# Performance work log

Measured on AMD Instinct MI355X. Metric: run time of the kernel, lower is better.

The kernel has to match this reference:

```python
import jax, jax.numpy as jnp
import numpy as np
from math import atanh

B, T, D_IN, H = 16, 1024, 512, 1024
INIT_A = atanh(0.95)


def setup_inputs() -> dict:
    key = jax.random.key(0)
    k1, k2, k3, k4 = jax.random.split(key, 4)
    x = jax.random.normal(k1, (B, T, D_IN), dtype=jnp.float32)
    h0 = jax.random.normal(k2, (B, H), dtype=jnp.float32)
    # raw_a initialized near atanh(0.95) as in the module, with small jitter
    raw_a = INIT_A + 0.01 * jax.random.normal(k3, (H,), dtype=jnp.float32)
    # xavier-uniform for W_x.weight [H, D_IN]
    limit = float(np.sqrt(6.0 / (D_IN + H)))
    W = jax.random.uniform(k4, (H, D_IN), dtype=jnp.float32, minval=-limit, maxval=limit)
    b = jnp.zeros((H,), dtype=jnp.float32)
    return {"x": x, "h0": h0, "raw_a": raw_a, "W": W, "b": b}


def reference(x, h0, raw_a, W, b):
    # h_t = a * h_{t-1} + W x_t + b, computed via cumprod/cumsum parallel-scan trick
    a = jnp.tanh(raw_a)                                   # [H] (rho is None)
    z = jnp.einsum('btd,hd->bth', x, W) + b               # [B,T,H]
    A = jnp.broadcast_to(a, (x.shape[1], a.shape[0]))     # [T,H]
    p = jnp.cumprod(A, axis=0)[None]                      # [1,T,H], p[t] = a^(t+1)
    v = jnp.cumsum(z / jnp.maximum(p, 1e-12), axis=1)     # [B,T,H]
    h = v * p + p * h0[:, None, :]                        # include initial state
    zero_mask = (jnp.abs(a) < 1e-6)[None, None, :]        # degenerate a ~ 0 channels
    h = jnp.where(zero_mask, z, h)
    return h
```

## Files before the change

### kernel.cpp

```cpp
#include <hip/hip_runtime.h>
#include <cstdint>

#define B_DIM 16
#define T_DIM 1024
#define DK    512
#define H_DIM 1024
#define CCH   16
#define LCH   64

typedef __bf16 bf16x8 __attribute__((ext_vector_type(8)));
typedef __bf16 bf16x4 __attribute__((ext_vector_type(4)));
typedef float  f32x4  __attribute__((ext_vector_type(4)));

typedef __attribute__((address_space(1))) unsigned int* as1p;
typedef __attribute__((address_space(3))) unsigned int* as3p;

__device__ __forceinline__ void async_cp16(const void* g, void* l) {
  __builtin_amdgcn_global_load_lds((as1p)(uint64_t)g,
                                   (as3p)(uint32_t)(uint64_t)l, 16, 0, 0);
}

__global__ __launch_bounds__(256) void cvt_f32_bf16(const float* __restrict__ in,
                                                    __bf16* __restrict__ out, int n4) {
  int i = blockIdx.x * 256 + threadIdx.x;
  if (i >= n4) return;
  f32x4 v = ((const f32x4*)in)[i];
  bf16x4 o;
  o.x = (__bf16)v.x; o.y = (__bf16)v.y; o.z = (__bf16)v.z; o.w = (__bf16)v.w;
  ((bf16x4*)out)[i] = o;
}

__global__ __launch_bounds__(256) void compute_meta(const float* __restrict__ raw_a,
                                                    float4* __restrict__ meta) {
  int h = blockIdx.x * 256 + threadIdx.x;
  if (h >= H_DIM) return;
  float a = tanhf(raw_a[h]);
  float la2 = log2f(fabsf(a));
  meta[h] = make_float4(a, la2, (a < 0.f) ? 1.f : 0.f, (fabsf(a) < 1e-6f) ? 1.f : 0.f);
}

__global__ __launch_bounds__(256) void gemm_bt(const __bf16* __restrict__ A,
                                               const __bf16* __restrict__ Bw,
                                               const float* __restrict__ bias,
                                               const float4* __restrict__ meta,
                                               float* __restrict__ C,
                                               float* __restrict__ S) {
  constexpr int N = H_DIM;
  constexpr int K = DK;

  __shared__ __align__(16) __bf16 As[128 * 32];
  __shared__ __align__(16) __bf16 Bs[128 * 32];
  __shared__ float sred[2][128];

  const int tid  = threadIdx.x;
  const int wave = tid >> 6;
  const int lane = tid & 63;
  const int m0 = blockIdx.y * 128;
  const int n0 = blockIdx.x * 128;
  const int wm = wave >> 1;
  const int wn = wave & 1;

  const int lrow = lane >> 2;
  const int lk   = (lane & 3) * 8;

  f32x4 acc[4][4];
#pragma unroll
  for (int i = 0; i < 4; ++i)
#pragma unroll
    for (int j = 0; j < 4; ++j) acc[i][j] = (f32x4){0.f, 0.f, 0.f, 0.f};

  for (int k0 = 0; k0 < K; k0 += 32) {
    __syncthreads();
#pragma unroll
    for (int q = 0; q < 2; ++q) {
      const int rbase = q * 64 + wave * 16;
      const __bf16* ga = A  + (size_t)(m0 + rbase + lrow) * K + k0 + lk;
      async_cp16(ga, As + rbase * 32);
      const __bf16* gb = Bw + (size_t)(n0 + rbase + lrow) * K + k0 + lk;
      async_cp16(gb, Bs + rbase * 32);
    }
    __syncthreads();
#pragma unroll
    for (int i = 0; i < 4; ++i) {
      const bf16x8 af = *(const bf16x8*)(As + (wm * 64 + i * 16 + (lane & 15)) * 32 + (lane >> 4) * 8);
#pragma unroll
      for (int j = 0; j < 4; ++j) {
        const bf16x8 bf = *(const bf16x8*)(Bs + (wn * 64 + j * 16 + (lane & 15)) * 32 + (lane >> 4) * 8);
        acc[i][j] = __builtin_amdgcn_mfma_f32_16x16x32_bf16(af, bf, acc[i][j], 0, 0, 0);
      }
    }
  }

  const int cl = lane & 15;
  const int rq = (lane >> 4) * 4;
  const int b = m0 >> 10;
  const int tloc0 = m0 & 1023;
#pragma unroll
  for (int j = 0; j < 4; ++j) {
    const int col = n0 + wn * 64 + j * 16 + cl;
    const float bv = bias[col];
    const float4 mt = meta[col];
    const float la2 = mt.y;
    const bool neg = mt.z != 0.f;
    float ssum = 0.f;
#pragma unroll
    for (int i = 0; i < 4; ++i) {
      const int rowg = wm * 64 + i * 16 + rq;
#pragma unroll
      for (int r = 0; r < 4; ++r) {
        const int tp1 = tloc0 + rowg + r + 1;
        const float zf = acc[i][j][r] + bv;
        C[(size_t)(m0 + rowg + r) * N + col] = zf;
        float inv = fminf(__builtin_amdgcn_exp2f(-la2 * (float)tp1), 1e12f);
        if (neg && (tp1 & 1)) inv = 1e12f;
        ssum += zf * inv;
      }
    }
    ssum += __shfl_xor(ssum, 16, 64);
    ssum += __shfl_xor(ssum, 32, 64);
    if ((lane >> 4) == 0) sred[wm][wn * 64 + j * 16 + cl] = ssum;
  }
  __syncthreads();
  {
    const int g = tid >> 7;
    const int col = tid & 127;
    S[((size_t)b * CCH + (tloc0 >> 6) + g) * H_DIM + n0 + col] = sred[g][col];
  }
}

__global__ __launch_bounds__(256) void scan_pass2(const float* __restrict__ z,
                                                  const float4* __restrict__ meta,
                                                  const float* __restrict__ S,
                                                  const float* __restrict__ h0,
                                                  float* __restrict__ out) {
  const int h = blockIdx.x * 256 + threadIdx.x;
  const int c = blockIdx.y;
  const int b = blockIdx.z;
  float prefix = 0.f;
  for (int cc = 0; cc < c; ++cc) prefix += S[((size_t)b * CCH + cc) * H_DIM + h];
  const float4 mt = meta[h];
  const float la2 = mt.y;
  const bool neg = mt.z != 0.f;
  const bool zm  = mt.w != 0.f;
  const float h0v = h0[(size_t)b * H_DIM + h];
  float v = prefix;
  const int t0 = c * LCH;
  const size_t base = ((size_t)b * T_DIM + t0) * H_DIM + h;
  for (int t = 0; t < LCH; ++t) {
    const float zt = z[base + (size_t)t * H_DIM];
    const int tp1 = t0 + t + 1;
    float pv = __builtin_amdgcn_exp2f(la2 * (float)tp1);
    if (neg && (tp1 & 1)) pv = -pv;
    const float pc = fmaxf(pv, 1e-12f);
    v += zt * __builtin_amdgcn_rcpf(pc);
    const float hv = v * pv + pv * h0v;
    out[base + (size_t)t * H_DIM] = zm ? zt : hv;
  }
}

extern "C" void kernel_launch(void* const* d_in, const int* in_sizes, int n_in,
                              void* d_out, int out_size, void* d_ws, size_t ws_size,
                              hipStream_t stream) {
  const float* x     = (const float*)d_in[0];
  const float* h0    = (const float*)d_in[1];
  const float* raw_a = (const float*)d_in[2];
  const float* W     = (const float*)d_in[3];
  const float* bias  = (const float*)d_in[4];
  float* out = (float*)d_out;

  char* ws = (char*)d_ws;
  float*  z    = (float*)(ws);
  __bf16* xb   = (__bf16*)(ws + 67108864);
  __bf16* wb   = (__bf16*)(ws + 67108864 + 16777216);
  float4* meta = (float4*)(ws + 67108864 + 16777216 + 1048576);
  float*  S    = (float*)(ws + 67108864 + 16777216 + 1048576 + 16384);

  cvt_f32_bf16<<<(B_DIM * T_DIM * DK / 4 + 255) / 256, 256, 0, stream>>>(x, xb, B_DIM * T_DIM * DK / 4);
  cvt_f32_bf16<<<(H_DIM * DK / 4 + 255) / 256, 256, 0, stream>>>(W, wb, H_DIM * DK / 4);
  compute_meta<<<H_DIM / 256, 256, 0, stream>>>(raw_a, meta);
  gemm_bt<<<dim3(H_DIM / 128, B_DIM * T_DIM / 128), 256, 0, stream>>>(xb, wb, bias, meta, z, S);
  scan_pass2<<<dim3(H_DIM / 256, CCH, B_DIM), 256, 0, stream>>>(z, meta, S, h0, out);
}
```

Measured before the change: 153.7 us.

## Fuse GEMM and chunked scan into one kernel with in-block carry

Replaces the separate GEMM (which wrote z and chunk sums) and scan pass with a single kernel where each block owns one batch and 32 hidden columns and walks the whole sequence in 256-step chunks, scanning the MFMA accumulators in registers with shuffles and carrying prefix sums through shared memory. This removes the 64 MB z round trip and a kernel launch. In exchange the grid shrinks to 512 blocks with narrow 32-column N tiles, so each block re-streams its x rows with little reuse of W and has a long serial time loop, which may cut MFMA efficiency and parallelism.

```diff
diff --git a/kernel.cpp b/kernel.cpp
--- a/kernel.cpp
+++ b/kernel.cpp
@@ -5,8 +5,6 @@
 #define T_DIM 1024
 #define DK    512
 #define H_DIM 1024
-#define CCH   16
-#define LCH   64
 
 typedef __bf16 bf16x8 __attribute__((ext_vector_type(8)));
 typedef __bf16 bf16x4 __attribute__((ext_vector_type(4)));
@@ -39,122 +37,148 @@
   meta[h] = make_float4(a, la2, (a < 0.f) ? 1.f : 0.f, (fabsf(a) < 1e-6f) ? 1.f : 0.f);
 }
 
-__global__ __launch_bounds__(256) void gemm_bt(const __bf16* __restrict__ A,
-                                               const __bf16* __restrict__ Bw,
-                                               const float* __restrict__ bias,
-                                               const float4* __restrict__ meta,
-                                               float* __restrict__ C,
-                                               float* __restrict__ S) {
-  constexpr int N = H_DIM;
-  constexpr int K = DK;
-
-  __shared__ __align__(16) __bf16 As[128 * 32];
-  __shared__ __align__(16) __bf16 Bs[128 * 32];
-  __shared__ float sred[2][128];
+__global__ __launch_bounds__(256, 2) void fused_rnn(const __bf16* __restrict__ xb,
+                                                    const __bf16* __restrict__ wb,
+                                                    const float* __restrict__ bias,
+                                                    const float4* __restrict__ meta,
+                                                    const float* __restrict__ h0g,
+                                                    float* __restrict__ out) {
+  __shared__ __align__(16) __bf16 As[256 * 32];
+  __shared__ __align__(16) __bf16 Bs[32 * 32];
+  __shared__ float chunkTot[4][32];
+  __shared__ float colCarry[32];
 
   const int tid  = threadIdx.x;
   const int wave = tid >> 6;
   const int lane = tid & 63;
-  const int m0 = blockIdx.y * 128;
-  const int n0 = blockIdx.x * 128;
-  const int wm = wave >> 1;
-  const int wn = wave & 1;
-
-  const int lrow = lane >> 2;
-  const int lk   = (lane & 3) * 8;
-
-  f32x4 acc[4][4];
-#pragma unroll
-  for (int i = 0; i < 4; ++i)
-#pragma unroll
-    for (int j = 0; j < 4; ++j) acc[i][j] = (f32x4){0.f, 0.f, 0.f, 0.f};
-
-  for (int k0 = 0; k0 < K; k0 += 32) {
+  const int q = lane >> 4;
+  const int c = lane & 15;
+
+  const int b    = blockIdx.x & 15;
+  const int n0   = (blockIdx.x >> 4) * 32;
+
+  float bias_j[2], la2_j[2], h0_j[2];
+  bool neg_j[2], zm_j[2];
+#pragma unroll
+  for (int j = 0; j < 2; ++j) {
+    const int col = n0 + j * 16 + c;
+    bias_j[j] = bias[col];
+    const float4 mt = meta[col];
+    la2_j[j] = mt.y;
+    neg_j[j] = mt.z != 0.f;
+    zm_j[j]  = mt.w != 0.f;
+    h0_j[j]  = h0g[(size_t)b * H_DIM + col];
+  }
+
+  if (tid < 32) colCarry[tid] = 0.f;
+
+  const int srow = lane >> 2;
+  const int skof = (lane & 3) * 8;
+
+  for (int mc = 0; mc < 4; ++mc) {
+    const int t0 = mc * 256;
+    const __bf16* Abase = xb + (size_t)(b * T_DIM + t0) * DK;
+
+    f32x4 acc[4][2];
+#pragma unroll
+    for (int i = 0; i < 4; ++i)
+#pragma unroll
+      for (int j = 0; j < 2; ++j) acc[i][j] = (f32x4){0.f, 0.f, 0.f, 0.f};
+
+    for (int k0 = 0; k0 < DK; k0 += 32) {
+      __syncthreads();
+#pragma unroll
+      for (int r = 0; r < 4; ++r) {
+        const int s = wave * 4 + r;
+        const __bf16* ga = Abase + (size_t)(s * 16 + srow) * DK + k0 + skof;
+        async_cp16(ga, As + s * 16 * 32);
+      }
+      if (wave < 2) {
+        const __bf16* gb = wb + (size_t)(n0 + wave * 16 + srow) * DK + k0 + skof;
+        async_cp16(gb, Bs + wave * 16 * 32);
+      }
+      __syncthreads();
+      bf16x8 af[4], bfr[2];
+#pragma unroll
+      for (int i = 0; i < 4; ++i)
+        af[i] = *(const bf16x8*)(As + (wave * 64 + i * 16 + c) * 32 + q * 8);
+#pragma unroll
+      for (int j = 0; j < 2; ++j)
+        bfr[j] = *(const bf16x8*)(Bs + (j * 16 + c) * 32 + q * 8);
+#pragma unroll
+      for (int i = 0; i < 4; ++i)
+#pragma unroll
+        for (int j = 0; j < 2; ++j)
+          acc[i][j] = __builtin_amdgcn_mfma_f32_16x16x32_bf16(af[i], bfr[j], acc[i][j], 0, 0, 0);
+    }
+
+    f32x4 vloc[4][2];
+    float icarry[2] = {0.f, 0.f};
+#pragma unroll
+    for (int i = 0; i < 4; ++i) {
+#pragma unroll
+      for (int j = 0; j < 2; ++j) {
+        const float la2 = la2_j[j];
+        f32x4 w;
+#pragma unroll
+        for (int r = 0; r < 4; ++r) {
+          const int tp1 = t0 + wave * 64 + i * 16 + q * 4 + r + 1;
+          const float z = acc[i][j][r] + bias_j[j];
+          float inv = fminf(__builtin_amdgcn_exp2f(-la2 * (float)tp1), 1e12f);
+          if (neg_j[j] && (tp1 & 1)) inv = 1e12f;
+          w[r] = z * inv;
+        }
+        const float pr0 = w[0];
+        const float pr1 = pr0 + w[1];
+        const float pr2 = pr1 + w[2];
+        const float pr3 = pr2 + w[3];
+        const float x1 = __shfl_xor(pr3, 16, 64);
+        const float x2 = __shfl_xor(pr3, 32, 64);
+        const float x3 = __shfl_xor(pr3, 48, 64);
+        float sq = 0.f;
+        if (q >= 2) sq += x2 + x3;
+        if (q & 1) sq += x1;
+        const float base = icarry[j] + sq;
+        vloc[i][j] = (f32x4){base + pr0, base + pr1, base + pr2, base + pr3};
+        icarry[j] += pr3 + x1 + x2 + x3;
+      }
+    }
+    if (q == 0) {
+#pragma unroll
+      for (int j = 0; j < 2; ++j) chunkTot[wave][j * 16 + c] = icarry[j];
+    }
     __syncthreads();
-#pragma unroll
-    for (int q = 0; q < 2; ++q) {
-      const int rbase = q * 64 + wave * 16;
-      const __bf16* ga = A  + (size_t)(m0 + rbase + lrow) * K + k0 + lk;
-      async_cp16(ga, As + rbase * 32);
-      const __bf16* gb = Bw + (size_t)(n0 + rbase + lrow) * K + k0 + lk;
-      async_cp16(gb, Bs + rbase * 32);
+
+    float cc[2];
+#pragma unroll
+    for (int j = 0; j < 2; ++j) {
+      float s = colCarry[j * 16 + c];
+      for (int w2 = 0; w2 < 4; ++w2)
+        if (w2 < wave) s += chunkTot[w2][j * 16 + c];
+      cc[j] = s;
+    }
+#pragma unroll
+    for (int i = 0; i < 4; ++i) {
+#pragma unroll
+      for (int j = 0; j < 2; ++j) {
+        const float la2 = la2_j[j];
+        const int col = n0 + j * 16 + c;
+#pragma unroll
+        for (int r = 0; r < 4; ++r) {
+          const int tl = t0 + wave * 64 + i * 16 + q * 4 + r;
+          const int tp1 = tl + 1;
+          float pv = __builtin_amdgcn_exp2f(la2 * (float)tp1);
+          if (neg_j[j] && (tp1 & 1)) pv = -pv;
+          const float v = cc[j] + vloc[i][j][r];
+          const float hv = pv * v + pv * h0_j[j];
+          const float zval = acc[i][j][r] + bias_j[j];
+          out[(size_t)(b * T_DIM + tl) * H_DIM + col] = zm_j[j] ? zval : hv;
+        }
+      }
     }
     __syncthreads();
-#pragma unroll
-    for (int i = 0; i < 4; ++i) {
-      const bf16x8 af = *(const bf16x8*)(As + (wm * 64 + i * 16 + (lane & 15)) * 32 + (lane >> 4) * 8);
-#pragma unroll
-      for (int j = 0; j < 4; ++j) {
-        const bf16x8 bf = *(const bf16x8*)(Bs + (wn * 64 + j * 16 + (lane & 15)) * 32 + (lane >> 4) * 8);
-        acc[i][j] = __builtin_amdgcn_mfma_f32_16x16x32_bf16(af, bf, acc[i][j], 0, 0, 0);
-      }
-    }
-  }
-
-  const int cl = lane & 15;
-  const int rq = (lane >> 4) * 4;
-  const int b = m0 >> 10;
-  const int tloc0 = m0 & 1023;
-#pragma unroll
-  for (int j = 0; j < 4; ++j) {
-    const int col = n0 + wn * 64 + j * 16 + cl;
-    const float bv = bias[col];
-    const float4 mt = meta[col];
-    const float la2 = mt.y;
-    const bool neg = mt.z != 0.f;
-    float ssum = 0.f;
-#pragma unroll
-    for (int i = 0; i < 4; ++i) {
-      const int rowg = wm * 64 + i * 16 + rq;
-#pragma unroll
-      for (int r = 0; r < 4; ++r) {
-        const int tp1 = tloc0 + rowg + r + 1;
-        const float zf = acc[i][j][r] + bv;
-        C[(size_t)(m0 + rowg + r) * N + col] = zf;
-        float inv = fminf(__builtin_amdgcn_exp2f(-la2 * (float)tp1), 1e12f);
-        if (neg && (tp1 & 1)) inv = 1e12f;
-        ssum += zf * inv;
-      }
-    }
-    ssum += __shfl_xor(ssum, 16, 64);
-    ssum += __shfl_xor(ssum, 32, 64);
-    if ((lane >> 4) == 0) sred[wm][wn * 64 + j * 16 + cl] = ssum;
-  }
-  __syncthreads();
-  {
-    const int g = tid >> 7;
-    const int col = tid & 127;
-    S[((size_t)b * CCH + (tloc0 >> 6) + g) * H_DIM + n0 + col] = sred[g][col];
-  }
-}
-
-__global__ __launch_bounds__(256) void scan_pass2(const float* __restrict__ z,
-                                                  const float4* __restrict__ meta,
-                                                  const float* __restrict__ S,
-                                                  const float* __restrict__ h0,
-                                                  float* __restrict__ out) {
-  const int h = blockIdx.x * 256 + threadIdx.x;
-  const int c = blockIdx.y;
-  const int b = blockIdx.z;
-  float prefix = 0.f;
-  for (int cc = 0; cc < c; ++cc) prefix += S[((size_t)b * CCH + cc) * H_DIM + h];
-  const float4 mt = meta[h];
-  const float la2 = mt.y;
-  const bool neg = mt.z != 0.f;
-  const bool zm  = mt.w != 0.f;
-  const float h0v = h0[(size_t)b * H_DIM + h];
-  float v = prefix;
-  const int t0 = c * LCH;
-  const size_t base = ((size_t)b * T_DIM + t0) * H_DIM + h;
-  for (int t = 0; t < LCH; ++t) {
-    const float zt = z[base + (size_t)t * H_DIM];
-    const int tp1 = t0 + t + 1;
-    float pv = __builtin_amdgcn_exp2f(la2 * (float)tp1);
-    if (neg && (tp1 & 1)) pv = -pv;
-    const float pc = fmaxf(pv, 1e-12f);
-    v += zt * __builtin_amdgcn_rcpf(pc);
-    const float hv = v * pv + pv * h0v;
-    out[base + (size_t)t * H_DIM] = zm ? zt : hv;
+    if (tid < 32)
+      colCarry[tid] += chunkTot[0][tid] + chunkTot[1][tid] + chunkTot[2][tid] + chunkTot[3][tid];
   }
 }
 
@@ -169,15 +193,12 @@
   float* out = (float*)d_out;
 
   char* ws = (char*)d_ws;
-  float*  z    = (float*)(ws);
-  __bf16* xb   = (__bf16*)(ws + 67108864);
-  __bf16* wb   = (__bf16*)(ws + 67108864 + 16777216);
-  float4* meta = (float4*)(ws + 67108864 + 16777216 + 1048576);
-  float*  S    = (float*)(ws + 67108864 + 16777216 + 1048576 + 16384);
+  __bf16* xb   = (__bf16*)(ws);
+  __bf16* wb   = (__bf16*)(ws + 16777216);
+  float4* meta = (float4*)(ws + 16777216 + 1048576);
 
   cvt_f32_bf16<<<(B_DIM * T_DIM * DK / 4 + 255) / 256, 256, 0, stream>>>(x, xb, B_DIM * T_DIM * DK / 4);
   cvt_f32_bf16<<<(H_DIM * DK / 4 + 255) / 256, 256, 0, stream>>>(W, wb, H_DIM * DK / 4);
   compute_meta<<<H_DIM / 256, 256, 0, stream>>>(raw_a, meta);
-  gemm_bt<<<dim3(H_DIM / 128, B_DIM * T_DIM / 128), 256, 0, stream>>>(xb, wb, bias, meta, z, S);
-  scan_pass2<<<dim3(H_DIM / 256, CCH, B_DIM), 256, 0, stream>>>(z, meta, S, h0, out);
-}
+  fused_rnn<<<512, 256, 0, stream>>>(xb, wb, bias, meta, h0, out);
+}
```

Result: faster. 146.7 us (-4.5%).
